# Optimization experiments

Measured on AMD Instinct MI355X. Metric: run time of the kernel, lower is better.

The kernel has to match this reference:

```python
import jax, jax.numpy as jnp
from jax import lax
import numpy as np

B, H, W, C = 4, 128, 128, 128   # C == d_route == n_heads, patch_len == H
OFFSET_RANGE = 5.0              # offset_range_factor == kernel == 5
SCALE = C ** -0.5               # self.scale_factor = d_route**-0.5
CYCLE = 168


def grid_sample_bilinear(img, grid):
    """torch.nn.functional.grid_sample(mode='bilinear', padding_mode='zeros', align_corners=False).
    img: (B,C,H,W); grid: (B,H,W,2) with (x,y) in [-1,1]."""
    Bn, Cn, Hn, Wn = img.shape
    xg = (grid[..., 0] + 1.0) * (Wn / 2.0) - 0.5
    yg = (grid[..., 1] + 1.0) * (Hn / 2.0) - 0.5
    x0 = jnp.floor(xg)
    y0 = jnp.floor(yg)
    img_flat = img.reshape(Bn, Cn, Hn * Wn)
    out = jnp.zeros_like(img)
    for xi in (x0, x0 + 1.0):
        for yi in (y0, y0 + 1.0):
            wgt = (1.0 - jnp.abs(xg - xi)) * (1.0 - jnp.abs(yg - yi))
            valid = (xi >= 0) & (xi <= Wn - 1) & (yi >= 0) & (yi <= Hn - 1)
            ix = jnp.clip(xi, 0, Wn - 1).astype(jnp.int32)
            iy = jnp.clip(yi, 0, Hn - 1).astype(jnp.int32)
            idx = (iy * Wn + ix).reshape(Bn, 1, -1)                      # (B,1,H*W)
            vals = jnp.take_along_axis(img_flat, idx, axis=2).reshape(Bn, Cn, Hn, Wn)
            out = out + vals * (wgt * valid.astype(img.dtype))[:, None, :, :]
    return out


def setup_inputs():
    key = jax.random.key(0)
    ks = jax.random.split(key, 12)
    s = C ** -0.5
    inp = {
        "x": jax.random.normal(ks[0], (B, H, W, C), dtype=jnp.float32),
        "cycle_index": jax.random.randint(ks[1], (B, 128), 0, CYCLE),  # dead path in cycle_mode='None'
        "Wq": jax.random.normal(ks[2], (C, C), dtype=jnp.float32) * s,
        "bq": jnp.zeros((C,), dtype=jnp.float32),
        "Wk": jax.random.normal(ks[3], (C, C), dtype=jnp.float32) * s,
        "bk": jnp.zeros((C,), dtype=jnp.float32),
        "Wv": jax.random.normal(ks[4], (C, C), dtype=jnp.float32) * s,
        "bv": jnp.zeros((C,), dtype=jnp.float32),
        "Wo": jax.random.normal(ks[5], (C, C), dtype=jnp.float32) * s,
        "bo": jnp.zeros((C,), dtype=jnp.float32),
        "Wc1": jax.random.normal(ks[6], (C, C, 5, 5), dtype=jnp.float32) * (1.0 / np.sqrt(C * 25)),
        "bc1": jnp.zeros((C,), dtype=jnp.float32),
        "Wc2": jax.random.normal(ks[7], (2, C), dtype=jnp.float32) * s,   # 1x1 conv, no bias
        "rel_bias": jax.random.normal(ks[8], (1, C, H, 1), dtype=jnp.float32) * 0.02,
    }
    return inp


def reference(x, cycle_index, Wq, bq, Wk, bk, Wv, bv, Wo, bo, Wc1, bc1, Wc2, rel_bias):
    Bn, Hn, Wn, Cn = x.shape
    xc = jnp.transpose(x, (0, 3, 1, 2))                                  # (B,C,H,W)
    # proj_q (1x1 conv) on x (cycle_mode='None')
    q = jnp.einsum('oc,bchw->bohw', Wq, xc) + bq[None, :, None, None]
    # proj_offset: 5x5 conv (pad 2) -> 1x1 conv to 2 channels, tanh * offset_range_factor
    c1 = lax.conv_general_dilated(q, Wc1, (1, 1), ((2, 2), (2, 2)),
                                  dimension_numbers=('NCHW', 'OIHW', 'NCHW')) + bc1[None, :, None, None]
    offset = jnp.tanh(jnp.einsum('oc,bchw->bohw', Wc2, c1)) * OFFSET_RANGE  # (B,2,H,W)
    # create_grid_like + normalize_grid (faithful, incl. x-coord normalized by H and vice versa)
    gx, gy = jnp.meshgrid(jnp.arange(Wn, dtype=x.dtype), jnp.arange(Hn, dtype=x.dtype), indexing='xy')
    grid = jnp.stack([gx, gy], axis=0)                                   # (2,H,W)
    vgrid = grid[None] + offset                                          # (B,2,H,W)
    gh = 2.0 * vgrid[:, 0] / max(Hn - 1, 1) - 1.0
    gw = 2.0 * vgrid[:, 1] / max(Wn - 1, 1) - 1.0
    sgrid = jnp.stack([gh, gw], axis=-1)                                 # (B,H,W,2) = (x,y) for grid_sample
    x_sampled = grid_sample_bilinear(xc, sgrid)                          # (B,C,H,W); n_groups=1 -> rearrange is identity
    k = (jnp.einsum('oc,bchw->bohw', Wk, x_sampled) + bk[None, :, None, None]).reshape(Bn * Cn, Hn, Wn)
    v = (jnp.einsum('oc,bchw->bohw', Wv, x_sampled) + bv[None, :, None, None] + rel_bias).reshape(Bn * Cn, Hn, Wn)
    qr = q.reshape(Bn * Cn, Hn, Wn)
    scores = jnp.einsum('bid,bjd->bij', qr, k) * SCALE                   # (B*C,H,H)
    attn = jax.nn.softmax(scores, axis=-1)
    out = jnp.einsum('bij,bjd->bid', attn, v)                            # (B*C,H,W)
    out = out.reshape(Bn, Hn, Wn, Cn)                                    # faithful raw reshape (as in original)
    return out @ Wo.T + bo
```

## Files before the change

### kernel.cpp

```cpp
#include <hip/hip_runtime.h>
#include <math.h>

#define IMG 16384

typedef short short4v __attribute__((ext_vector_type(4)));
typedef short short8  __attribute__((ext_vector_type(8)));
typedef float floatx4 __attribute__((ext_vector_type(4)));

__device__ __forceinline__ float4 ld4(const float* p) {
    return *reinterpret_cast<const float4*>(p);
}
__device__ __forceinline__ short f2bf(float f) {
    union { float f; unsigned u; } v; v.f = f;
    unsigned r = v.u + 0x7fffu + ((v.u >> 16) & 1u);
    return (short)(r >> 16);
}
__device__ __forceinline__ float bf2f(short s) {
    union { unsigned u; float f; } v;
    v.u = ((unsigned)(unsigned short)s) << 16;
    return v.f;
}

__launch_bounds__(256)
__global__ void k_wprep(const float* __restrict__ Wc1, const float* __restrict__ Wc2,
                        const float* __restrict__ bc1, const float* __restrict__ Wq,
                        const float* __restrict__ bq, const float* __restrict__ Wk,
                        const float* __restrict__ Wv, const float* __restrict__ Wo,
                        float* __restrict__ W2, float* __restrict__ cst,
                        float* __restrict__ b_eff, short* __restrict__ wbf,
                        short* __restrict__ w2h, short* __restrict__ w2l) {
    const int t = threadIdx.x;
    if (blockIdx.x >= 50) {
        if (blockIdx.x == 50) {
            for (int i = t; i < 14 * 128; i += 256) {
                w2h[6400 + i] = 0;
                w2l[6400 + i] = 0;
            }
        }
        int i = (blockIdx.x - 50) * 256 + t;
        int base = i * 8;
        int sel = base >> 14, off = base & 16383;
        const float* s = (sel == 0) ? Wq : (sel == 1) ? Wk : (sel == 2) ? Wv : Wo;
        float4 a = ld4(s + off), b = ld4(s + off + 4);
        short8 o;
        o[0] = f2bf(a.x); o[1] = f2bf(a.y); o[2] = f2bf(a.z); o[3] = f2bf(a.w);
        o[4] = f2bf(b.x); o[5] = f2bf(b.y); o[6] = f2bf(b.z); o[7] = f2bf(b.w);
        *reinterpret_cast<short8*>(wbf + base) = o;
        return;
    }
    __shared__ float U[128];
    __shared__ float red[256];
    __shared__ float wc2[128];
    __shared__ float bql[128];
    const int tt = blockIdx.x;
    const int tch = tt / 25, tap = tt % 25;
    if (t < 128) { wc2[t] = Wc2[tch * 128 + t]; bql[t] = bq[t]; }
    __syncthreads();
    const int c = t & 127, half = t >> 7;
    float p = 0.f;
    for (int o = half * 64; o < half * 64 + 64; ++o)
        p += wc2[o] * Wc1[(o * 128 + c) * 25 + tap];
    red[half * 128 + c] = p;
    __syncthreads();
    if (t < 128) U[t] = red[t] + red[128 + t];
    __syncthreads();
    float p2 = 0.f;
    for (int cc = half * 64; cc < half * 64 + 64; ++cc)
        p2 += U[cc] * Wq[cc * 128 + c];
    red[half * 128 + c] = p2;
    __syncthreads();
    if (t < 128) {
        float vv = red[t] + red[128 + t];
        W2[tt * 128 + t] = vv;
        short hh = f2bf(vv);
        w2h[tt * 128 + t] = hh;
        w2l[tt * 128 + t] = f2bf(vv - bf2f(hh));
    }
    if (t < 128) red[t] = U[t] * bql[t];
    __syncthreads();
    if (t == 0) {
        float s = 0.f;
        for (int j = 0; j < 128; ++j) s += red[j];
        cst[tt] = s;
    }
    if (tap == 0) {
        __syncthreads();
        if (t < 128) red[t] = wc2[t] * bc1[t];
        __syncthreads();
        if (t == 0) {
            float s = 0.f;
            for (int j = 0; j < 128; ++j) s += red[j];
            b_eff[tch] = s;
        }
    }
}

__launch_bounds__(256, 2)
__global__ void k_off(const float* __restrict__ x, const short* __restrict__ w2h,
                      const short* __restrict__ w2l, const float* __restrict__ cst,
                      float* __restrict__ P, short* __restrict__ x_bf) {
    __shared__ __align__(16) float stage[64 * 132];
    const int t = threadIdx.x;
    const int w = t >> 6, l = t & 63, l15 = l & 15, quad = l >> 4;
    const int p0 = blockIdx.x * 128;
    const int b = p0 >> 14, pix0 = p0 & (IMG - 1);

    floatx4 acc[2][4];
#pragma unroll
    for (int im = 0; im < 2; ++im)
#pragma unroll
        for (int in = 0; in < 4; ++in) acc[im][in] = (floatx4){0.f, 0.f, 0.f, 0.f};

    const float* xb = x + (size_t)p0 * 128;
    short* xbb = x_bf + (size_t)p0 * 128;

#pragma unroll
    for (int kc = 0; kc < 128; kc += 32) {
        short8 ah[2], al[2];
#pragma unroll
        for (int im = 0; im < 2; ++im) {
            int row = w * 32 + im * 16 + l15;
            const float* src = xb + row * 128 + kc + quad * 8;
            float4 f0 = ld4(src), f1 = ld4(src + 4);
            float fv[8] = {f0.x, f0.y, f0.z, f0.w, f1.x, f1.y, f1.z, f1.w};
            short8 h8, l8;
#pragma unroll
            for (int r = 0; r < 8; ++r) {
                short hh = f2bf(fv[r]);
                h8[r] = hh;
                l8[r] = f2bf(fv[r] - bf2f(hh));
            }
            ah[im] = h8; al[im] = l8;
            *reinterpret_cast<short8*>(xbb + row * 128 + kc + quad * 8) = h8;
        }
        short8 bh[4], bl[4];
#pragma unroll
        for (int in = 0; in < 4; ++in) {
            int o = in * 16 + l15;
            bh[in] = *reinterpret_cast<const short8*>(w2h + o * 128 + kc + quad * 8);
            bl[in] = *reinterpret_cast<const short8*>(w2l + o * 128 + kc + quad * 8);
        }
#pragma unroll
        for (int im = 0; im < 2; ++im)
#pragma unroll
            for (int in = 0; in < 4; ++in) {
                acc[im][in] = __builtin_amdgcn_mfma_f32_16x16x32_bf16(
                    ah[im], bh[in], acc[im][in], 0, 0, 0);
                acc[im][in] = __builtin_amdgcn_mfma_f32_16x16x32_bf16(
                    ah[im], bl[in], acc[im][in], 0, 0, 0);
                acc[im][in] = __builtin_amdgcn_mfma_f32_16x16x32_bf16(
                    al[im], bh[in], acc[im][in], 0, 0, 0);
            }
    }
#pragma unroll
    for (int im = 0; im < 2; ++im)
#pragma unroll
        for (int in = 0; in < 4; ++in) {
            int o = in * 16 + l15;
            int row0 = w * 32 + im * 16 + quad * 4;
            *reinterpret_cast<float4*>(&stage[o * 132 + row0]) =
                make_float4(acc[im][in][0], acc[im][in][1],
                            acc[im][in][2], acc[im][in][3]);
        }
    __syncthreads();
    for (int id = t; id < 50 * 32; id += 256) {
        int o = id >> 5, px4 = (id & 31) * 4;
        float c = cst[o];
        float4 v = *reinterpret_cast<float4*>(&stage[o * 132 + px4]);
        v.x += c; v.y += c; v.z += c; v.w += c;
        *reinterpret_cast<float4*>(P + ((size_t)(b * 50 + o)) * IMG + pix0 + px4) = v;
    }
}

__launch_bounds__(256, 2)
__global__ void k_fused3(const float* __restrict__ P, const float* __restrict__ b_eff,
                         const short* __restrict__ x_bf, const short* __restrict__ wbf,
                         const float* __restrict__ bq, const float* __restrict__ bk,
                         const float* __restrict__ bv, const float* __restrict__ rel,
                         short* __restrict__ q_bf, short* __restrict__ k_bf,
                         short* __restrict__ v_bf) {
    __shared__ __align__(16) char smem[70656];
    float* rowsP  = (float*)smem;
    short* stg    = (short*)smem;
    short* xsT    = (short*)(smem + 34816);
    float* offs_l = (float*)(smem + 69632);

    const int t = threadIdx.x;
    const int w = t >> 6, l = t & 63, l15 = l & 15, quad = l >> 4;
    const int mh = w >> 1, nh = w & 1;
    const int bh = blockIdx.x;
    const int b = bh >> 7, h = bh & 127;

    for (int id = t; id < 1600; id += 256) {
        int o = id >> 5, q4 = (id & 31) * 4;
        int di = (o % 25) / 5;
        int r = h + di - 2;
        int rc = min(max(r, 0), 127);
        float4 v = ld4(P + ((size_t)(b * 50 + o)) * IMG + rc * 128 + q4);
        float m = (r >= 0 && r < 128) ? 1.f : 0.f;
        v.x *= m; v.y *= m; v.z *= m; v.w *= m;
        *reinterpret_cast<float4*>(&rowsP[o * 136 + 4 + q4]) = v;
    }
    for (int id = t; id < 400; id += 256) {
        int o = id >> 3, c = id & 7;
        rowsP[o * 136 + (c < 4 ? c : 128 + c)] = 0.f;
    }
    __syncthreads();
    {
        int wp = t & 127, tc = t >> 7;
        float acc = 0.f;
#pragma unroll
        for (int di = 0; di < 5; ++di)
#pragma unroll
            for (int dj = 0; dj < 5; ++dj)
                acc += rowsP[(tc * 25 + di * 5 + dj) * 136 + wp + dj + 2];
        offs_l[tc * 128 + wp] = tanhf(acc + b_eff[tc]) * 5.0f;
    }
    __syncthreads();

    {
        const short* xbase = x_bf + (size_t)b * IMG * 128;
#pragma unroll
        for (int it = 0; it < 8; ++it) {
            int id = t + it * 256;
            int px = id >> 4, c8 = id & 15;
            float ox = offs_l[px];
            float oy = offs_l[128 + px];
            float xg = ((float)px + ox) * (128.0f / 127.0f) - 0.5f;
            float yg = ((float)h  + oy) * (128.0f / 127.0f) - 0.5f;
            float x0f = floorf(xg), y0f = floorf(yg);
            float fx = xg - x0f, fy = yg - y0f;
            int x0 = (int)x0f, y0 = (int)y0f;
            float s[8];
#pragma unroll
            for (int r = 0; r < 8; ++r) s[r] = 0.f;
#pragma unroll
            for (int tap = 0; tap < 4; ++tap) {
                int xi = x0 + (tap & 1), yi = y0 + (tap >> 1);
                float wgt = ((tap & 1) ? fx : 1.f - fx) * ((tap >> 1) ? fy : 1.f - fy);
                wgt = (xi >= 0 && xi < 128 && yi >= 0 && yi < 128) ? wgt : 0.f;
                int xc = min(max(xi, 0), 127), yc = min(max(yi, 0), 127);
                short8 v = *reinterpret_cast<const short8*>(
                    xbase + ((size_t)(yc * 128 + xc)) * 128 + c8 * 8);
#pragma unroll
                for (int r = 0; r < 8; ++r) s[r] = fmaf(wgt, bf2f(v[r]), s[r]);
            }
            short8 o;
#pragma unroll
            for (int r = 0; r < 8; ++r) o[r] = f2bf(s[r]);
            *reinterpret_cast<short8*>(&xsT[px * 136 + c8 * 8]) = o;
        }
    }

    {
        const short* xr = x_bf + ((size_t)(b * 128 + h)) * 128 * 128;
        floatx4 acc[4][4];
#pragma unroll
        for (int im = 0; im < 4; ++im)
#pragma unroll
            for (int in = 0; in < 4; ++in)
                acc[im][in] = (floatx4){0.f, 0.f, 0.f, 0.f};
#pragma unroll
        for (int kc = 0; kc < 128; kc += 32) {
            short8 af[4], bf_[4];
#pragma unroll
            for (int im = 0; im < 4; ++im)
                af[im] = *reinterpret_cast<const short8*>(
                    xr + (mh * 64 + im * 16 + l15) * 128 + kc + quad * 8);
#pragma unroll
            for (int in = 0; in < 4; ++in)
                bf_[in] = *reinterpret_cast<const short8*>(
                    wbf + (nh * 64 + in * 16 + l15) * 128 + kc + quad * 8);
#pragma unroll
            for (int im = 0; im < 4; ++im)
#pragma unroll
                for (int in = 0; in < 4; ++in)
                    acc[im][in] = __builtin_amdgcn_mfma_f32_16x16x32_bf16(
                        af[im], bf_[in], acc[im][in], 0, 0, 0);
        }
        __syncthreads();
#pragma unroll
        for (int in = 0; in < 4; ++in) {
            int o = nh * 64 + in * 16 + l15;
            float bb = bq[o];
#pragma unroll
            for (int im = 0; im < 4; ++im) {
                int row0 = mh * 64 + im * 16 + quad * 4;
                short4v s = {f2bf(acc[im][in][0] + bb), f2bf(acc[im][in][1] + bb),
                             f2bf(acc[im][in][2] + bb), f2bf(acc[im][in][3] + bb)};
                *reinterpret_cast<short4v*>(&stg[o * 136 + row0]) = s;
            }
        }
    }
    __syncthreads();
    for (int id = t; id < 2048; id += 256) {
        int o = id >> 4, seg = id & 15;
        *reinterpret_cast<short8*>(
            q_bf + ((size_t)(b * 128 + o)) * IMG + h * 128 + seg * 8)
            = *reinterpret_cast<const short8*>(&stg[o * 136 + seg * 8]);
    }

    {
        floatx4 ak[4][4], av[4][4];
#pragma unroll
        for (int im = 0; im < 4; ++im)
#pragma unroll
            for (int in = 0; in < 4; ++in) {
                ak[im][in] = (floatx4){0.f, 0.f, 0.f, 0.f};
                av[im][in] = (floatx4){0.f, 0.f, 0.f, 0.f};
            }
#pragma unroll
        for (int kc = 0; kc < 128; kc += 32) {
            short8 af[4], bk_[4], bv_[4];
#pragma unroll
            for (int im = 0; im < 4; ++im)
                af[im] = *reinterpret_cast<const short8*>(
                    &xsT[(mh * 64 + im * 16 + l15) * 136 + kc + quad * 8]);
#pragma unroll
            for (int in = 0; in < 4; ++in) {
                bk_[in] = *reinterpret_cast<const short8*>(
                    wbf + 16384 + (nh * 64 + in * 16 + l15) * 128 + kc + quad * 8);
                bv_[in] = *reinterpret_cast<const short8*>(
                    wbf + 32768 + (nh * 64 + in * 16 + l15) * 128 + kc + quad * 8);
            }
#pragma unroll
            for (int im = 0; im < 4; ++im)
#pragma unroll
                for (int in = 0; in < 4; ++in) {
                    ak[im][in] = __builtin_amdgcn_mfma_f32_16x16x32_bf16(
                        af[im], bk_[in], ak[im][in], 0, 0, 0);
                    av[im][in] = __builtin_amdgcn_mfma_f32_16x16x32_bf16(
                        af[im], bv_[in], av[im][in], 0, 0, 0);
                }
        }
        __syncthreads();
#pragma unroll
        for (int in = 0; in < 4; ++in) {
            int o = nh * 64 + in * 16 + l15;
            float bbk = bk[o];
            float bbv = bv[o] + rel[o * 128 + h];
#pragma unroll
            for (int im = 0; im < 4; ++im) {
                int row0 = mh * 64 + im * 16 + quad * 4;
                short4v sk = {f2bf(ak[im][in][0] + bbk), f2bf(ak[im][in][1] + bbk),
                              f2bf(ak[im][in][2] + bbk), f2bf(ak[im][in][3] + bbk)};
                short4v sv = {f2bf(av[im][in][0] + bbv), f2bf(av[im][in][1] + bbv),
                              f2bf(av[im][in][2] + bbv), f2bf(av[im][in][3] + bbv)};
                *reinterpret_cast<short4v*>(&stg[o * 136 + row0]) = sk;
                *reinterpret_cast<short4v*>(&xsT[o * 136 + row0]) = sv;
            }
        }
    }
    __syncthreads();
    for (int id = t; id < 4096; id += 256) {
        int sel = id >> 11;
        int o = (id >> 4) & 127, seg = id & 15;
        short* dst = sel ? v_bf : k_bf;
        const short* src = sel ? xsT : stg;
        *reinterpret_cast<short8*>(
            dst + ((size_t)(b * 128 + o)) * IMG + h * 128 + seg * 8)
            = *reinterpret_cast<const short8*>(&src[o * 136 + seg * 8]);
    }
}

__launch_bounds__(256, 2)
__global__ void k_attn3(const short* __restrict__ q_bf, const short* __restrict__ k_bf,
                        const short* __restrict__ v_bf, const short* __restrict__ WoB,
                        const float* __restrict__ bo, float* __restrict__ outp) {
    __shared__ __align__(16) char smem[71680];
    short* Pb   = (short*)smem;
    short* vT   = (short*)(smem + 34816);
    float* Ystg = (float*)smem;
    float* redm = (float*)(smem + 69632);
    float* reds = (float*)(smem + 70656);

    const int t = threadIdx.x;
    const int w = t >> 6, l = t & 63, l15 = l & 15, quad = l >> 4;
    const int mh = w >> 1, nh = w & 1;
    const size_t hb = (size_t)blockIdx.x * IMG;
    const short* qp = q_bf + hb;
    const short* kp = k_bf + hb;
    const short* vp = v_bf + hb;

    for (int id = t; id < 512; id += 256) {
        int j4 = id >> 4, seg = id & 15;
        const short* src = vp + (j4 * 4) * 128 + seg * 8;
        short8 v0 = *reinterpret_cast<const short8*>(src);
        short8 v1 = *reinterpret_cast<const short8*>(src + 128);
        short8 v2 = *reinterpret_cast<const short8*>(src + 256);
        short8 v3 = *reinterpret_cast<const short8*>(src + 384);
        int phys = (((j4 >> 1) ^ seg) & 15) * 8 + (j4 & 1) * 4;
#pragma unroll
        for (int r = 0; r < 8; ++r) {
            short4v wv = {v0[r], v1[r], v2[r], v3[r]};
            *reinterpret_cast<short4v*>(&vT[(seg * 8 + r) * 136 + phys]) = wv;
        }
    }

    floatx4 acc[4][4];
#pragma unroll
    for (int im = 0; im < 4; ++im)
#pragma unroll
        for (int in = 0; in < 4; ++in)
            acc[im][in] = (floatx4){0.f, 0.f, 0.f, 0.f};

#pragma unroll
    for (int kc = 0; kc < 128; kc += 32) {
        short8 af[4], bf_[4];
#pragma unroll
        for (int im = 0; im < 4; ++im)
            af[im] = *reinterpret_cast<const short8*>(
                qp + (mh * 64 + im * 16 + l15) * 128 + kc + quad * 8);
#pragma unroll
        for (int in = 0; in < 4; ++in)
            bf_[in] = *reinterpret_cast<const short8*>(
                kp + (nh * 64 + in * 16 + l15) * 128 + kc + quad * 8);
#pragma unroll
        for (int im = 0; im < 4; ++im)
#pragma unroll
            for (int in = 0; in < 4; ++in)
                acc[im][in] = __builtin_amdgcn_mfma_f32_16x16x32_bf16(
                    af[im], bf_[in], acc[im][in], 0, 0, 0);
    }

    const float scale = 0.08838834764831845f;
    float mloc[4][4];
#pragma unroll
    for (int im = 0; im < 4; ++im)
#pragma unroll
        for (int r = 0; r < 4; ++r) {
            float m = acc[im][0][r];
#pragma unroll
            for (int in = 1; in < 4; ++in) m = fmaxf(m, acc[im][in][r]);
            mloc[im][r] = m;
        }
#pragma unroll
    for (int mask = 1; mask < 16; mask <<= 1)
#pragma unroll
        for (int im = 0; im < 4; ++im)
#pragma unroll
            for (int r = 0; r < 4; ++r)
                mloc[im][r] = fmaxf(mloc[im][r], __shfl_xor(mloc[im][r], mask, 64));
    if (l15 == 0) {
#pragma unroll
        for (int im = 0; im < 4; ++im)
#pragma unroll
            for (int r = 0; r < 4; ++r)
                redm[nh * 128 + mh * 64 + im * 16 + quad * 4 + r] = mloc[im][r];
    }
    __syncthreads();
    float sloc[4][4];
#pragma unroll
    for (int im = 0; im < 4; ++im)
#pragma unroll
        for (int r = 0; r < 4; ++r) {
            int row = mh * 64 + im * 16 + quad * 4 + r;
            float m = fmaxf(redm[row], redm[128 + row]);
            float ss = 0.f;
#pragma unroll
            for (int in = 0; in < 4; ++in) {
                float e = __expf((acc[im][in][r] - m) * scale);
                acc[im][in][r] = e;
                ss += e;
            }
            sloc[im][r] = ss;
        }
#pragma unroll
    for (int mask = 1; mask < 16; mask <<= 1)
#pragma unroll
        for (int im = 0; im < 4; ++im)
#pragma unroll
            for (int r = 0; r < 4; ++r)
                sloc[im][r] += __shfl_xor(sloc[im][r], mask, 64);
    if (l15 == 0) {
#pragma unroll
        for (int im = 0; im < 4; ++im)
#pragma unroll
            for (int r = 0; r < 4; ++r)
                reds[nh * 128 + mh * 64 + im * 16 + quad * 4 + r] = sloc[im][r];
    }
    __syncthreads();
#pragma unroll
    for (int im = 0; im < 4; ++im)
#pragma unroll
        for (int r = 0; r < 4; ++r) {
            int row = mh * 64 + im * 16 + quad * 4 + r;
            float inv = 1.0f / (reds[row] + reds[128 + row]);
#pragma unroll
            for (int in = 0; in < 4; ++in) {
                int col = nh * 64 + in * 16 + l15;
                Pb[row * 136 + col] = f2bf(acc[im][in][r] * inv);
            }
        }
    __syncthreads();

#pragma unroll
    for (int im = 0; im < 4; ++im)
#pragma unroll
        for (int in = 0; in < 4; ++in)
            acc[im][in] = (floatx4){0.f, 0.f, 0.f, 0.f};
#pragma unroll
    for (int kc = 0; kc < 128; kc += 32) {
        short8 af[4], bf_[4];
#pragma unroll
        for (int im = 0; im < 4; ++im)
            af[im] = *reinterpret_cast<const short8*>(
                &Pb[(mh * 64 + im * 16 + l15) * 136 + kc + quad * 8]);
#pragma unroll
        for (int in = 0; in < 4; ++in) {
            int dRow = nh * 64 + in * 16 + l15;
            int cphys = (((kc >> 3) + quad) ^ (dRow >> 3)) & 15;
            bf_[in] = *reinterpret_cast<const short8*>(
                &vT[dRow * 136 + cphys * 8]);
        }
#pragma unroll
        for (int im = 0; im < 4; ++im)
#pragma unroll
            for (int in = 0; in < 4; ++in)
                acc[im][in] = __builtin_amdgcn_mfma_f32_16x16x32_bf16(
                    af[im], bf_[in], acc[im][in], 0, 0, 0);
    }
    __syncthreads();
#pragma unroll
    for (int im = 0; im < 4; ++im)
#pragma unroll
        for (int in = 0; in < 4; ++in) {
            int col = nh * 64 + in * 16 + l15;
#pragma unroll
            for (int r = 0; r < 4; ++r) {
                int row = mh * 64 + im * 16 + quad * 4 + r;
                Pb[row * 136 + col] = f2bf(acc[im][in][r]);
            }
        }
    __syncthreads();

    float bb[4];
#pragma unroll
    for (int in = 0; in < 4; ++in) bb[in] = bo[nh * 64 + in * 16 + l15];
#pragma unroll
    for (int im = 0; im < 4; ++im)
#pragma unroll
        for (int in = 0; in < 4; ++in)
            acc[im][in] = (floatx4){0.f, 0.f, 0.f, 0.f};
#pragma unroll
    for (int kc = 0; kc < 128; kc += 32) {
        short8 af[4], bf_[4];
#pragma unroll
        for (int im = 0; im < 4; ++im)
            af[im] = *reinterpret_cast<const short8*>(
                &Pb[(mh * 64 + im * 16 + l15) * 136 + kc + quad * 8]);
#pragma unroll
        for (int in = 0; in < 4; ++in)
            bf_[in] = *reinterpret_cast<const short8*>(
                WoB + (nh * 64 + in * 16 + l15) * 128 + kc + quad * 8);
#pragma unroll
        for (int im = 0; im < 4; ++im)
#pragma unroll
            for (int in = 0; in < 4; ++in)
                acc[im][in] = __builtin_amdgcn_mfma_f32_16x16x32_bf16(
                    af[im], bf_[in], acc[im][in], 0, 0, 0);
    }
    __syncthreads();
#pragma unroll
    for (int im = 0; im < 4; ++im)
#pragma unroll
        for (int in = 0; in < 4; ++in) {
            int col = nh * 64 + in * 16 + l15;
#pragma unroll
            for (int r = 0; r < 4; ++r) {
                int row = mh * 64 + im * 16 + quad * 4 + r;
                Ystg[row * 132 + col] = acc[im][in][r] + bb[in];
            }
        }
    __syncthreads();
    for (int id = t; id < 4096; id += 256) {
        int row = id >> 5, c4 = (id & 31) * 4;
        *reinterpret_cast<float4*>(outp + hb + (size_t)row * 128 + c4) =
            *reinterpret_cast<const float4*>(&Ystg[row * 132 + c4]);
    }
}

extern "C" void kernel_launch(void* const* d_in, const int* in_sizes, int n_in,
                              void* d_out, int out_size, void* d_ws, size_t ws_size,
                              hipStream_t stream) {
    const float* x   = (const float*)d_in[0];
    const float* Wq  = (const float*)d_in[2];
    const float* bq  = (const float*)d_in[3];
    const float* Wk  = (const float*)d_in[4];
    const float* bk  = (const float*)d_in[5];
    const float* Wv  = (const float*)d_in[6];
    const float* bv  = (const float*)d_in[7];
    const float* Wo  = (const float*)d_in[8];
    const float* bo  = (const float*)d_in[9];
    const float* Wc1 = (const float*)d_in[10];
    const float* bc1 = (const float*)d_in[11];
    const float* Wc2 = (const float*)d_in[12];
    const float* rel = (const float*)d_in[13];

    char* wsb = (char*)d_ws;
    short* q_bf  = (short*)(wsb);
    short* k_bf  = (short*)(wsb + 1ull * 16777216);
    short* v_bf  = (short*)(wsb + 2ull * 16777216);
    short* x_bf  = (short*)(wsb + 3ull * 16777216);
    float* P     = (float*)(wsb + 4ull * 16777216);
    float* W2    = (float*)(wsb + 4ull * 16777216 + 13107200);
    float* cst   = W2 + 6400;
    float* b_eff = cst + 64;
    short* wbf   = (short*)(b_eff + 16);
    short* w2h   = wbf + 65536;
    short* w2l   = w2h + 8192;
    float* outp  = (float*)d_out;

    hipLaunchKernelGGL(k_wprep,  dim3(82),   dim3(256), 0, stream, Wc1, Wc2, bc1, Wq, bq,
                       Wk, Wv, Wo, W2, cst, b_eff, wbf, w2h, w2l);
    hipLaunchKernelGGL(k_off,    dim3(512),  dim3(256), 0, stream, x, w2h, w2l, cst, P, x_bf);
    hipLaunchKernelGGL(k_fused3, dim3(512),  dim3(256), 0, stream, P, b_eff, x_bf, wbf,
                       bq, bk, bv, rel, q_bf, k_bf, v_bf);
    hipLaunchKernelGGL(k_attn3,  dim3(512),  dim3(256), 0, stream, q_bf, k_bf, v_bf,
                       wbf + 49152, bo, outp);
}
```

Baseline: 197.7 us.

## Fold output projection Wo into V before attention

Uses associativity (P·V)·Wo^T = P·(V·Wo^T) to apply the Wo projection to V inside the fused QKV kernel, which removes one GEMM stage and its LDS round trip from the attention kernel. The attention kernel now writes P·V' plus the bias directly. In exchange the fused kernel does an extra MFMA GEMM and adds an extra bf16 rounding of the pre-multiplied V, and the raw-reshape semantics must line up with the plane and row indexing for the result to stay correct.

```diff
diff --git a/kernel.cpp b/kernel.cpp
--- a/kernel.cpp
+++ b/kernel.cpp
@@ -352,20 +352,64 @@
         }
     }
     __syncthreads();
-    for (int id = t; id < 4096; id += 256) {
-        int sel = id >> 11;
-        int o = (id >> 4) & 127, seg = id & 15;
-        short* dst = sel ? v_bf : k_bf;
-        const short* src = sel ? xsT : stg;
+    for (int id = t; id < 2048; id += 256) {
+        int o = id >> 4, seg = id & 15;
         *reinterpret_cast<short8*>(
-            dst + ((size_t)(b * 128 + o)) * IMG + h * 128 + seg * 8)
-            = *reinterpret_cast<const short8*>(&src[o * 136 + seg * 8]);
+            k_bf + ((size_t)(b * 128 + o)) * IMG + h * 128 + seg * 8)
+            = *reinterpret_cast<const short8*>(&stg[o * 136 + seg * 8]);
+    }
+
+    {
+        const short* WoB = wbf + 49152;
+        floatx4 aw[4][4];
+#pragma unroll
+        for (int im = 0; im < 4; ++im)
+#pragma unroll
+            for (int in = 0; in < 4; ++in)
+                aw[im][in] = (floatx4){0.f, 0.f, 0.f, 0.f};
+#pragma unroll
+        for (int kc = 0; kc < 128; kc += 32) {
+            short8 af[4], bf_[4];
+#pragma unroll
+            for (int im = 0; im < 4; ++im)
+                af[im] = *reinterpret_cast<const short8*>(
+                    WoB + (mh * 64 + im * 16 + l15) * 128 + kc + quad * 8);
+#pragma unroll
+            for (int in = 0; in < 4; ++in)
+                bf_[in] = *reinterpret_cast<const short8*>(
+                    &xsT[(nh * 64 + in * 16 + l15) * 136 + kc + quad * 8]);
+#pragma unroll
+            for (int im = 0; im < 4; ++im)
+#pragma unroll
+                for (int in = 0; in < 4; ++in)
+                    aw[im][in] = __builtin_amdgcn_mfma_f32_16x16x32_bf16(
+                        af[im], bf_[in], aw[im][in], 0, 0, 0);
+        }
+        __syncthreads();
+#pragma unroll
+        for (int in = 0; in < 4; ++in) {
+            int plane = nh * 64 + in * 16 + l15;
+#pragma unroll
+            for (int im = 0; im < 4; ++im) {
+                int row0 = mh * 64 + im * 16 + quad * 4;
+                short4v s = {f2bf(aw[im][in][0]), f2bf(aw[im][in][1]),
+                             f2bf(aw[im][in][2]), f2bf(aw[im][in][3])};
+                *reinterpret_cast<short4v*>(&stg[plane * 136 + row0]) = s;
+            }
+        }
+    }
+    __syncthreads();
+    for (int id = t; id < 2048; id += 256) {
+        int o = id >> 4, seg = id & 15;
+        *reinterpret_cast<short8*>(
+            v_bf + ((size_t)(b * 128 + o)) * IMG + h * 128 + seg * 8)
+            = *reinterpret_cast<const short8*>(&stg[o * 136 + seg * 8]);
     }
 }
 
 __launch_bounds__(256, 2)
 __global__ void k_attn3(const short* __restrict__ q_bf, const short* __restrict__ k_bf,
-                        const short* __restrict__ v_bf, const short* __restrict__ WoB,
+                        const short* __restrict__ v_bf,
                         const float* __restrict__ bo, float* __restrict__ outp) {
     __shared__ __align__(16) char smem[71680];
     short* Pb   = (short*)smem;
@@ -494,6 +538,9 @@
         }
     __syncthreads();
 
+    float bb[4];
+#pragma unroll
+    for (int in = 0; in < 4; ++in) bb[in] = bo[nh * 64 + in * 16 + l15];
 #pragma unroll
     for (int im = 0; im < 4; ++im)
 #pragma unroll
@@ -513,46 +560,6 @@
             bf_[in] = *reinterpret_cast<const short8*>(
                 &vT[dRow * 136 + cphys * 8]);
         }
-#pragma unroll
-        for (int im = 0; im < 4; ++im)
-#pragma unroll
-            for (int in = 0; in < 4; ++in)
-                acc[im][in] = __builtin_amdgcn_mfma_f32_16x16x32_bf16(
-                    af[im], bf_[in], acc[im][in], 0, 0, 0);
-    }
-    __syncthreads();
-#pragma unroll
-    for (int im = 0; im < 4; ++im)
-#pragma unroll
-        for (int in = 0; in < 4; ++in) {
-            int col = nh * 64 + in * 16 + l15;
-#pragma unroll
-            for (int r = 0; r < 4; ++r) {
-                int row = mh * 64 + im * 16 + quad * 4 + r;
-                Pb[row * 136 + col] = f2bf(acc[im][in][r]);
-            }
-        }
-    __syncthreads();
-
-    float bb[4];
-#pragma unroll
-    for (int in = 0; in < 4; ++in) bb[in] = bo[nh * 64 + in * 16 + l15];
-#pragma unroll
-    for (int im = 0; im < 4; ++im)
-#pragma unroll
-        for (int in = 0; in < 4; ++in)
-            acc[im][in] = (floatx4){0.f, 0.f, 0.f, 0.f};
-#pragma unroll
-    for (int kc = 0; kc < 128; kc += 32) {
-        short8 af[4], bf_[4];
-#pragma unroll
-        for (int im = 0; im < 4; ++im)
-            af[im] = *reinterpret_cast<const short8*>(
-                &Pb[(mh * 64 + im * 16 + l15) * 136 + kc + quad * 8]);
-#pragma unroll
-        for (int in = 0; in < 4; ++in)
-            bf_[in] = *reinterpret_cast<const short8*>(
-                WoB + (nh * 64 + in * 16 + l15) * 128 + kc + quad * 8);
 #pragma unroll
         for (int im = 0; im < 4; ++im)
 #pragma unroll
@@ -617,5 +624,5 @@
     hipLaunchKernelGGL(k_fused3, dim3(512),  dim3(256), 0, stream, P, b_eff, x_bf, wbf,
                        bq, bk, bv, rel, q_bf, k_bf, v_bf);
     hipLaunchKernelGGL(k_attn3,  dim3(512),  dim3(256), 0, stream, q_bf, k_bf, v_bf,
-                       wbf + 49152, bo, outp);
-}
+                       bo, outp);
+}
```

Result: no change. 198.1 us (+0.2%).
